# Performance work log

Measured on AMD Instinct MI355X. Metric: run time of the kernel, lower is better.

Reference implementation:

```python
import jax, jax.numpy as jnp
from jax import lax
import numpy as np

L = 4
KH, KW = 3, 3


def setup_inputs() -> dict:
    key = jax.random.key(0)
    k1, k2, k3, k4 = jax.random.split(key, 4)
    B, H, W, C = 32, 512, 512, 3
    inputs = jax.random.normal(k1, (B, H, W, C), dtype=jnp.float32)
    # posterior_loc ~ 'random_normal' initializer (stddev 0.05 in keras)
    posterior_loc = 0.05 * jax.random.normal(k2, (KH, KW, C, 1), dtype=jnp.float32)
    # posterior_scale initialized to constant -5.0 (small perturbation for non-degeneracy)
    posterior_scale = jnp.full((KH, KW, C, 1), -5.0, dtype=jnp.float32) + 0.1 * jax.random.normal(k3, (KH, KW, C, 1), dtype=jnp.float32)
    # reparameterization noise, one independent sample per pyramid level
    eps = jax.random.normal(k4, (L, KH, KW, C, 1), dtype=jnp.float32)
    return {"inputs": inputs, "posterior_loc": posterior_loc, "posterior_scale": posterior_scale, "eps": eps}


def _center_mask(dtype):
    # zero at the kernel center, one elsewhere (scatter of sampled values into non-center taps)
    m = np.ones((KH, KW, 1, 1), dtype=np.float32)
    m[KH // 2, KW // 2, 0, 0] = 0.0
    return jnp.asarray(m, dtype=dtype)


def _depthwise(x, kernel_hwc1):
    # x: [B,h,w,C], kernel_hwc1: [KH,KW,C,1] (TF depthwise layout) -> HWIO [KH,KW,1,C]
    C = x.shape[-1]
    k = jnp.transpose(kernel_hwc1, (0, 1, 3, 2))
    return lax.conv_general_dilated(
        x, k, window_strides=(1, 1), padding="SAME",
        dimension_numbers=("NHWC", "HWIO", "NHWC"), feature_group_count=C)


def reference(inputs, posterior_loc, posterior_scale, eps):
    B, H, W, C = inputs.shape
    sigma = jax.nn.softplus(posterior_scale)  # posterior stddev
    mask = _center_mask(inputs.dtype)
    total_error = jnp.zeros((B, H, W), dtype=inputs.dtype)
    for l in range(1, L + 1):
        factor = 2 ** (l - 1)
        th, tw = H // factor, W // factor
        ds = jax.image.resize(inputs, (B, th, tw, C), method="bilinear", antialias=True)
        # sampled Bayesian kernel: center tap zeroed, then normalized per channel
        v = posterior_loc + sigma * eps[l - 1]
        kern = v * mask
        kern = kern / (jnp.sum(kern, axis=(0, 1), keepdims=True) + 1e-7)
        r_hat = _depthwise(ds, kern)
        err = ds - r_hat
        up = jax.image.resize(err, (B, H, W, C), method="bilinear", antialias=False)
        total_error = total_error + jnp.sum(up, axis=-1)
    recon = jnp.mean(jnp.sum(jnp.square(total_error), axis=(1, 2)))
    # KL(N(mu, sigma) || N(0,1)), summed; added once per conv call -> L times
    kl = jnp.sum(-jnp.log(sigma) + 0.5 * (jnp.square(sigma) + jnp.square(posterior_loc)) - 0.5)
    return recon + L * kl
```

## Files before the change

kernel.cpp:

```cpp
#include <hip/hip_runtime.h>
#include <hip/hip_fp16.h>
#include <math.h>

#define BB 32
#define HH 512
#define WW 512
#define CC 3
#define LL 4

static __device__ __forceinline__ float softplusf_(float x) {
    if (x > 20.f) return x;
    return log1pf(expf(x));
}
static __device__ __forceinline__ int iclamp_(int v, int lo, int hi) {
    return v < lo ? lo : (v > hi ? hi : v);
}

__global__ void prep_kernel(const float* __restrict__ loc, const float* __restrict__ scale,
                            const float* __restrict__ eps, float* __restrict__ knorm,
                            double* __restrict__ kl_out) {
    int tid = threadIdx.x;
    float klv = 0.f;
    if (tid < 27) {
        float s = softplusf_(scale[tid]);
        float m = loc[tid];
        klv = -logf(s) + 0.5f * (s * s + m * m) - 0.5f;
    }
    #pragma unroll
    for (int off = 32; off; off >>= 1) klv += __shfl_down(klv, off);
    if (tid == 0) *kl_out = (double)klv;
    if (tid < 12) {
        int l = tid / 3;
        int c = tid - l * 3;
        float v[9];
        float sum = 0.f;
        #pragma unroll
        for (int t = 0; t < 9; ++t) {
            int idx = t * 3 + c;
            float s = softplusf_(scale[idx]);
            float val = loc[idx] + s * eps[l * 27 + idx];
            if (t == 4) val = 0.f;
            v[t] = val;
            sum += val;
        }
        float denom = sum + 1e-7f;
        #pragma unroll
        for (int t = 0; t < 9; ++t)
            knorm[l * 27 + t * 3 + c] = v[t] / denom;
    }
}

#define SJ(j) ((j) + ((j) >> 5))
#define PSTRIDE 532
#define RESC 1.1428571428571428f

__global__ void hpass_kernel(const float* __restrict__ x, __half* __restrict__ xh2,
                             __half* __restrict__ xh4, __half* __restrict__ xh8) {
    __shared__ __align__(16) float planes[4 * 3 * PSTRIDE];
    const int tid = threadIdx.x;
    const int lane = tid & 63;
    const int wv = tid >> 6;
    const int bh = blockIdx.x * 4 + wv;
    float* pl = planes + wv * (3 * PSTRIDE);

    const float4* src = (const float4*)(x + bh * (WW * CC));
    #pragma unroll
    for (int s = 0; s < 6; ++s) {
        int i = lane + (s << 6);
        float4 v = src[i];
        int g = i << 2;
        int j = g / 3;
        int c = g - j * 3;
        float e[4] = {v.x, v.y, v.z, v.w};
        #pragma unroll
        for (int u = 0; u < 4; ++u) {
            pl[c * PSTRIDE + SJ(j)] = e[u];
            ++c;
            if (c == 3) { c = 0; ++j; }
        }
    }
    asm volatile("s_waitcnt lgkmcnt(0)" ::: "memory");

    if (xh2) {
        const float W2k[4] = {0.125f, 0.375f, 0.375f, 0.125f};
        __half* o2 = xh2 + bh * 768;
        #pragma unroll
        for (int s = 0; s < 4; ++s) {
            int ow = lane + (s << 6);
            int j0 = 2 * ow - 1;
            bool edge = (j0 < 0) | (j0 + 3 > 511);
            float sc = edge ? RESC : 1.f;
            float wk[4]; int jj[4];
            #pragma unroll
            for (int k = 0; k < 4; ++k) {
                int j = j0 + k;
                wk[k] = (((unsigned)j < 512u) ? W2k[k] : 0.f) * sc;
                jj[k] = SJ(iclamp_(j, 0, 511));
            }
            #pragma unroll
            for (int c = 0; c < 3; ++c) {
                const float* p = pl + c * PSTRIDE;
                float a = 0.f;
                #pragma unroll
                for (int k = 0; k < 4; ++k) a += wk[k] * p[jj[k]];
                o2[ow * 3 + c] = __float2half_rn(a);
            }
        }
    }
    if (xh4) {
        const float W4k[8] = {0.03125f, 0.09375f, 0.15625f, 0.21875f,
                              0.21875f, 0.15625f, 0.09375f, 0.03125f};
        __half* o4 = xh4 + bh * 384;
        #pragma unroll
        for (int s = 0; s < 2; ++s) {
            int ow = lane + (s << 6);
            int j0 = 4 * ow - 2;
            bool edge = (j0 < 0) | (j0 + 7 > 511);
            float sc = edge ? RESC : 1.f;
            float wk[8]; int jj[8];
            #pragma unroll
            for (int k = 0; k < 8; ++k) {
                int j = j0 + k;
                wk[k] = (((unsigned)j < 512u) ? W4k[k] : 0.f) * sc;
                jj[k] = SJ(iclamp_(j, 0, 511));
            }
            #pragma unroll
            for (int c = 0; c < 3; ++c) {
                const float* p = pl + c * PSTRIDE;
                float a = 0.f;
                #pragma unroll
                for (int k = 0; k < 8; ++k) a += wk[k] * p[jj[k]];
                o4[ow * 3 + c] = __float2half_rn(a);
            }
        }
    }
    if (xh8) {
        const float W8k[16] = {0.0078125f, 0.0234375f, 0.0390625f, 0.0546875f,
                               0.0703125f, 0.0859375f, 0.1015625f, 0.1171875f,
                               0.1171875f, 0.1015625f, 0.0859375f, 0.0703125f,
                               0.0546875f, 0.0390625f, 0.0234375f, 0.0078125f};
        __half* o8 = xh8 + bh * 192;
        int ow = lane;
        int j0 = 8 * ow - 4;
        bool edge = (j0 < 0) | (j0 + 15 > 511);
        float sc = edge ? RESC : 1.f;
        float wk[16]; int jj[16];
        #pragma unroll
        for (int k = 0; k < 16; ++k) {
            int j = j0 + k;
            wk[k] = (((unsigned)j < 512u) ? W8k[k] : 0.f) * sc;
            jj[k] = SJ(iclamp_(j, 0, 511));
        }
        #pragma unroll
        for (int c = 0; c < 3; ++c) {
            const float* p = pl + c * PSTRIDE;
            float a = 0.f;
            #pragma unroll
            for (int k = 0; k < 16; ++k) a += wk[k] * p[jj[k]];
            o8[ow * 3 + c] = __float2half_rn(a);
        }
    }
}

template <int F, int THB>
static __device__ __forceinline__ void level_body(const __half* __restrict__ xh,
                                                  const float* __restrict__ knorm_all, int lvl,
                                                  float* __restrict__ es, int bx, int by, int b,
                                                  char* smem_raw) {
    constexpr int TH = HH / F, TW = WW / F, TW3 = TW * 3, TAPS = 2 * F;
    constexpr int RS = (THB + 3) * F;
    constexpr int DR = THB + 2;
    __half* stg = (__half*)smem_raw;
    float* dst = (float*)(smem_raw + RS * 108 * 2);
    float* wvv = dst + DR * 108;
    float* kn = wvv + DR * TAPS;
    int owb = bx * 32, ohb = by * THB;
    int tid = threadIdx.x;
    if (tid < 27) kn[tid] = knorm_all[lvl * 27 + tid];
    if (tid >= 32 && tid < 32 + DR) {
        int r = tid - 32;
        int oh = ohb - 1 + r;
        if (oh < 0 || oh >= TH) {
            #pragma unroll
            for (int k = 0; k < TAPS; ++k) wvv[r * TAPS + k] = 0.f;
        } else {
            float sfh = (oh + 0.5f) * F - 0.5f;
            int j0 = oh * F - F / 2;
            float tmp[TAPS]; float s = 0.f;
            #pragma unroll
            for (int k = 0; k < TAPS; ++k) {
                int j = j0 + k;
                float w = (j >= 0 && j < HH) ? (1.f - fabsf(j - sfh) * (1.0f / F)) : 0.f;
                tmp[k] = w; s += w;
            }
            float inv = 1.f / s;
            #pragma unroll
            for (int k = 0; k < TAPS; ++k) wvv[r * TAPS + k] = tmp[k] * inv;
        }
    }
    int jmin = (ohb - 1) * F - F / 2;
    int cb = owb * 3 - 4;
    bool fast = (cb >= 0) && (cb + 108 <= TW3);
    const __half* xb = xh + b * (HH * TW3);
    for (int i = tid; i < RS * 27; i += 256) {
        int r = i / 27;
        int c4 = (i - r * 27) * 4;
        int jh = iclamp_(jmin + r, 0, HH - 1);
        const __half* rp = xb + jh * TW3;
        if (fast) {
            *(ushort4*)&stg[r * 108 + c4] = *(const ushort4*)(rp + cb + c4);
        } else {
            #pragma unroll
            for (int u = 0; u < 4; ++u) {
                int col = iclamp_(cb + c4 + u, 0, TW3 - 1);
                stg[r * 108 + c4 + u] = rp[col];
            }
        }
    }
    __syncthreads();
    for (int i = tid; i < DR * 27; i += 256) {
        int r = i / 27;
        int c4 = (i - r * 27) * 4;
        int gc = cb + c4;
        float v0 = 0, v1 = 0, v2 = 0, v3 = 0;
        if ((unsigned)gc < (unsigned)TW3) {
            const __half* sp = &stg[r * F * 108 + c4];
            const float* wr = &wvv[r * TAPS];
            #pragma unroll
            for (int k = 0; k < TAPS; ++k) {
                float wk = wr[k];
                const __half2* h2 = (const __half2*)(sp + k * 108);
                float2 f0 = __half22float2(h2[0]);
                float2 f1 = __half22float2(h2[1]);
                v0 += wk * f0.x; v1 += wk * f0.y;
                v2 += wk * f1.x; v3 += wk * f1.y;
            }
        }
        float4 q; q.x = v0; q.y = v1; q.z = v2; q.w = v3;
        *(float4*)&dst[r * 108 + c4] = q;
    }
    __syncthreads();
    for (int i = tid; i < THB * 32; i += 256) {
        int wl = i & 31, hl = i >> 5;
        int base = hl * 108 + wl * 3 + 1;
        float e = 0.f;
        #pragma unroll
        for (int c = 0; c < 3; ++c) {
            float conv = 0.f;
            #pragma unroll
            for (int dh = 0; dh < 3; ++dh)
                #pragma unroll
                for (int dw = 0; dw < 3; ++dw)
                    conv += kn[(dh * 3 + dw) * 3 + c] * dst[base + dh * 108 + dw * 3 + c];
            e += dst[base + 108 + 3 + c] - conv;
        }
        es[b * (TH * TW) + (ohb + hl) * TW + owb + wl] = e;
    }
}

__global__ void levels_kernel(const __half* __restrict__ xh2, const __half* __restrict__ xh4,
                              const __half* __restrict__ xh8, const float* __restrict__ knorm,
                              float* __restrict__ es2, float* __restrict__ es3,
                              float* __restrict__ es4, int block_base) {
    __shared__ __align__(16) char smem[16896];
    int vb = blockIdx.x + block_base;
    if (vb < 4096) {
        level_body<2, 16>(xh2, knorm, 1, es2, vb & 7, (vb >> 3) & 15, vb >> 7, smem);
    } else if (vb < 6144) {
        int l = vb - 4096;
        level_body<4, 8>(xh4, knorm, 2, es3, l & 3, (l >> 2) & 15, l >> 6, smem);
    } else {
        int l = vb - 6144;
        level_body<8, 4>(xh8, knorm, 3, es4, l & 1, (l >> 1) & 15, l >> 5, smem);
    }
}

#define FPS 35
#define FPC (34 * FPS)
__global__ void __launch_bounds__(256, 8)
fused_kernel(const float* __restrict__ x, const float* __restrict__ knorm,
             const float* __restrict__ es2, const float* __restrict__ es3,
             const float* __restrict__ es4, double* __restrict__ partials) {
    __shared__ __align__(16) float planes[3 * FPC];
    __shared__ float e2t[18 * 19];
    __shared__ float e3t[10 * 11];
    __shared__ float e4t[6 * 7];
    __shared__ float kn[27];
    __shared__ float smf[4];
    int b = blockIdx.z;
    int hb = blockIdx.y * 32, wb = blockIdx.x * 32;
    int tid = threadIdx.x;
    if (tid < 27) kn[tid] = knorm[tid];
    const float* xb = x + b * (HH * WW * CC);
    int cb = wb * 3 - 4;
    bool fastc = (cb >= 0) && (cb + 108 <= WW * CC);
    for (int i = tid; i < 918; i += 256) {
        int r = i / 27;
        int f0 = (i - r * 27) * 4;
        int gh = hb - 1 + r;
        bool ghv = (unsigned)gh < (unsigned)HH;
        float vv[4] = {0.f, 0.f, 0.f, 0.f};
        if (ghv) {
            const float* rp = xb + gh * (WW * CC);
            if (fastc) {
                float4 v = *(const float4*)(rp + cb + f0);
                vv[0] = v.x; vv[1] = v.y; vv[2] = v.z; vv[3] = v.w;
            } else {
                int g0 = cb + f0;
                #pragma unroll
                for (int u = 0; u < 4; ++u)
                    vv[u] = ((unsigned)(g0 + u) < (unsigned)(WW * CC)) ? rp[g0 + u] : 0.f;
            }
        }
        #pragma unroll
        for (int u = 0; u < 4; ++u) {
            int f = f0 + u;
            if (f >= 1 && f <= 102) {
                int lc = (f - 1) / 3;
                int ch = (f - 1) - lc * 3;
                planes[ch * FPC + r * FPS + lc] = vv[u];
            }
        }
    }
    {
        const float* e2b = es2 + b * (256 * 256);
        int h0 = hb / 2 - 1, w0 = wb / 2 - 1;
        for (int i = tid; i < 18 * 32; i += 256) {
            int r = i >> 5, c = i & 31;
            if (c < 18) {
                int gh = iclamp_(h0 + r, 0, 255);
                int gw = iclamp_(w0 + c, 0, 255);
                e2t[r * 19 + c] = e2b[gh * 256 + gw];
            }
        }
        const float* e3b = es3 + b * (128 * 128);
        int h03 = hb / 4 - 1, w03 = wb / 4 - 1;
        if (tid < 160) {
            int r = tid >> 4, c = tid & 15;
            if (c < 10) {
                int gh = iclamp_(h03 + r, 0, 127);
                int gw = iclamp_(w03 + c, 0, 127);
                e3t[r * 11 + c] = e3b[gh * 128 + gw];
            }
        }
        const float* e4b = es4 + b * (64 * 64);
        int h04 = hb / 8 - 1, w04 = wb / 8 - 1;
        if (tid < 48) {
            int r = tid >> 3, c = tid & 7;
            if (c < 6) {
                int gh = iclamp_(h04 + r, 0, 63);
                int gw = iclamp_(w04 + c, 0, 63);
                e4t[r * 7 + c] = e4b[gh * 64 + gw];
            }
        }
    }
    __syncthreads();

    int q = tid >> 3;
    int a = tid & 7;
    float cv0 = 0, cv1 = 0, cv2 = 0, cv3 = 0;
    float ce0 = 0, ce1 = 0, ce2 = 0, ce3 = 0;
    #pragma unroll
    for (int c = 0; c < 3; ++c) {
        const float* P = planes + c * FPC;
        #pragma unroll
        for (int dh = 0; dh < 3; ++dh) {
            const float* r0 = P + (q + dh) * FPS + 4 * a;
            float w0 = r0[0], w1 = r0[1], w2 = r0[2], w3 = r0[3], w4 = r0[4], w5 = r0[5];
            float ka = kn[dh * 9 + c], kb = kn[dh * 9 + 3 + c], kc = kn[dh * 9 + 6 + c];
            cv0 += ka * w0 + kb * w1 + kc * w2;
            cv1 += ka * w1 + kb * w2 + kc * w3;
            cv2 += ka * w2 + kb * w3 + kc * w4;
            cv3 += ka * w3 + kb * w4 + kc * w5;
            if (dh == 1) { ce0 += w1; ce1 += w2; ce2 += w3; ce3 += w4; }
        }
    }
    float e[4] = {ce0 - cv0, ce1 - cv1, ce2 - cv2, ce3 - cv3};

    int n2 = q & 1;   float fh2 = n2 ? 0.25f : 0.75f;               int rh2 = (q >> 1) + n2;
    int n4 = q & 3;   float fh4 = ((n4 + 2) & 3) * 0.25f + 0.125f;  int rh4 = (q >> 2) + (n4 < 2 ? 0 : 1);
    int n8 = q & 7;   float fh8 = ((n8 + 4) & 7) * 0.125f + 0.0625f; int rh8 = (q >> 3) + (n8 < 4 ? 0 : 1);
    {
        const float* r0 = &e2t[rh2 * 19 + 2 * a];
        const float* r1 = r0 + 19;
        float t0 = r0[0], t1 = r0[1], t2 = r0[2], t3 = r0[3];
        float b0 = r1[0], b1 = r1[1], b2 = r1[2], b3 = r1[3];
        float top, bot;
        top = t0 + 0.75f * (t1 - t0); bot = b0 + 0.75f * (b1 - b0); e[0] += top + fh2 * (bot - top);
        top = t1 + 0.25f * (t2 - t1); bot = b1 + 0.25f * (b2 - b1); e[1] += top + fh2 * (bot - top);
        top = t1 + 0.75f * (t2 - t1); bot = b1 + 0.75f * (b2 - b1); e[2] += top + fh2 * (bot - top);
        top = t2 + 0.25f * (t3 - t2); bot = b2 + 0.25f * (b3 - b2); e[3] += top + fh2 * (bot - top);
    }
    {
        const float* r0 = &e3t[rh4 * 11 + a];
        const float* r1 = r0 + 11;
        float t0 = r0[0], t1 = r0[1], t2 = r0[2];
        float b0 = r1[0], b1 = r1[1], b2 = r1[2];
        float top, bot;
        top = t0 + 0.625f * (t1 - t0); bot = b0 + 0.625f * (b1 - b0); e[0] += top + fh4 * (bot - top);
        top = t0 + 0.875f * (t1 - t0); bot = b0 + 0.875f * (b1 - b0); e[1] += top + fh4 * (bot - top);
        top = t1 + 0.125f * (t2 - t1); bot = b1 + 0.125f * (b2 - b1); e[2] += top + fh4 * (bot - top);
        top = t1 + 0.375f * (t2 - t1); bot = b1 + 0.375f * (b2 - b1); e[3] += top + fh4 * (bot - top);
    }
    {
        int rw8 = (a >> 1) + (a & 1);
        const float* r0 = &e4t[rh8 * 7 + rw8];
        const float* r1 = r0 + 7;
        float t0 = r0[0], t1 = r0[1];
        float b0 = r1[0], b1 = r1[1];
        float fwb = (a & 1) ? 0.0625f : 0.5625f;
        #pragma unroll
        for (int p = 0; p < 4; ++p) {
            float fw = fwb + 0.125f * p;
            float top = t0 + fw * (t1 - t0);
            float bot = b0 + fw * (b1 - b0);
            e[p] += top + fh8 * (bot - top);
        }
    }
    float acc = e[0] * e[0] + e[1] * e[1] + e[2] * e[2] + e[3] * e[3];
    #pragma unroll
    for (int off = 32; off; off >>= 1) acc += __shfl_down(acc, off);
    if ((tid & 63) == 0) smf[tid >> 6] = acc;
    __syncthreads();
    if (tid == 0) {
        double s = (double)smf[0] + (double)smf[1] + (double)smf[2] + (double)smf[3];
        partials[(b * 16 + blockIdx.y) * 16 + blockIdx.x] = s;
    }
}

__global__ void final_kernel(const double* __restrict__ partials, int n,
                             const double* __restrict__ kl, float* __restrict__ out) {
    __shared__ double sm[1024];
    double acc = 0.0;
    for (int i = threadIdx.x; i < n; i += 1024) acc += partials[i];
    sm[threadIdx.x] = acc;
    __syncthreads();
    for (int s = 512; s > 0; s >>= 1) {
        if (threadIdx.x < (unsigned)s) sm[threadIdx.x] += sm[threadIdx.x + s];
        __syncthreads();
    }
    if (threadIdx.x == 0) out[0] = (float)(sm[0] / (double)BB + (double)LL * kl[0]);
}

extern "C" void kernel_launch(void* const* d_in, const int* in_sizes, int n_in,
                              void* d_out, int out_size, void* d_ws, size_t ws_size,
                              hipStream_t stream) {
    const float* x = (const float*)d_in[0];
    const float* loc = (const float*)d_in[1];
    const float* scale = (const float*)d_in[2];
    const float* eps = (const float*)d_in[3];
    float* out = (float*)d_out;

    char* ws = (char*)d_ws;
    float* knorm = (float*)(ws + 0);
    double* kl = (double*)(ws + 512);
    double* partials = (double*)(ws + 1024);
    float* es4 = (float*)(ws + 131072);
    float* es3 = (float*)(ws + 655360);
    float* es2 = (float*)(ws + 2752512);
    (void)in_sizes; (void)n_in; (void)out_size;

    prep_kernel<<<1, 64, 0, stream>>>(loc, scale, eps, knorm, kl);

    const size_t SINGLE_NEED = 55181312ull;
    if (ws_size >= SINGLE_NEED) {
        __half* xh2 = (__half*)(ws + 11141120);
        __half* xh4 = (__half*)(ws + 36306944);
        __half* xh8 = (__half*)(ws + 48889856);
        hpass_kernel<<<BB * HH / 4, 256, 0, stream>>>(x, xh2, xh4, xh8);
        levels_kernel<<<7168, 256, 0, stream>>>(xh2, xh4, xh8, knorm, es2, es3, es4, 0);
    } else {
        __half* xh4 = (__half*)(ws + 11141120);
        __half* xh8 = (__half*)(ws + 23724032);
        __half* xh2 = (__half*)(ws + 11141120);
        hpass_kernel<<<BB * HH / 4, 256, 0, stream>>>(x, nullptr, xh4, xh8);
        levels_kernel<<<3072, 256, 0, stream>>>(nullptr, xh4, xh8, knorm, es2, es3, es4, 4096);
        hpass_kernel<<<BB * HH / 4, 256, 0, stream>>>(x, xh2, nullptr, nullptr);
        levels_kernel<<<4096, 256, 0, stream>>>(xh2, nullptr, nullptr, knorm, es2, es3, es4, 0);
    }

    fused_kernel<<<dim3(16, 16, BB), 256, 0, stream>>>(x, knorm, es2, es3, es4, partials);
    final_kernel<<<1, 1024, 0, stream>>>(partials, 8192, kl, out);
}
```

Measured before the change: 109.6 us.

## Load full-res conv window directly from global; widen level staging loads to 16B

The fused kernel no longer stages the full-resolution input tile into shared-memory channel planes. Each thread now reads its 3x3 neighborhood rows straight from global memory with float4 loads and computes the depthwise conv in registers. This removes a large shared-memory allocation and a transposing scatter, which should raise occupancy, at the cost of redundant global and L2 reads across neighboring rows. The levels kernel staging also moves from 8-byte to 16-byte loads, with the row pitch padded to 112 halves and realigned offsets.

```diff
diff --git a/kernel.cpp b/kernel.cpp
--- a/kernel.cpp
+++ b/kernel.cpp
@@ -171,7 +171,7 @@
     constexpr int RS = (THB + 3) * F;
     constexpr int DR = THB + 2;
     __half* stg = (__half*)smem_raw;
-    float* dst = (float*)(smem_raw + RS * 108 * 2);
+    float* dst = (float*)(smem_raw + RS * 112 * 2);
     float* wvv = dst + DR * 108;
     float* kn = wvv + DR * TAPS;
     int owb = bx * 32, ohb = by * THB;
@@ -200,20 +200,21 @@
     }
     int jmin = (ohb - 1) * F - F / 2;
     int cb = owb * 3 - 4;
-    bool fast = (cb >= 0) && (cb + 108 <= TW3);
+    int cb2 = cb - 4;
+    bool fast = (cb2 >= 0) && (cb2 + 112 <= TW3);
     const __half* xb = xh + b * (HH * TW3);
-    for (int i = tid; i < RS * 27; i += 256) {
-        int r = i / 27;
-        int c4 = (i - r * 27) * 4;
+    for (int i = tid; i < RS * 14; i += 256) {
+        int r = i / 14;
+        int c8 = (i - r * 14) * 8;
         int jh = iclamp_(jmin + r, 0, HH - 1);
         const __half* rp = xb + jh * TW3;
         if (fast) {
-            *(ushort4*)&stg[r * 108 + c4] = *(const ushort4*)(rp + cb + c4);
+            *(uint4*)&stg[r * 112 + c8] = *(const uint4*)(rp + cb2 + c8);
         } else {
             #pragma unroll
-            for (int u = 0; u < 4; ++u) {
-                int col = iclamp_(cb + c4 + u, 0, TW3 - 1);
-                stg[r * 108 + c4 + u] = rp[col];
+            for (int u = 0; u < 8; ++u) {
+                int col = iclamp_(cb2 + c8 + u, 0, TW3 - 1);
+                stg[r * 112 + c8 + u] = rp[col];
             }
         }
     }
@@ -224,12 +225,12 @@
         int gc = cb + c4;
         float v0 = 0, v1 = 0, v2 = 0, v3 = 0;
         if ((unsigned)gc < (unsigned)TW3) {
-            const __half* sp = &stg[r * F * 108 + c4];
+            const __half* sp = &stg[r * F * 112 + c4 + 4];
             const float* wr = &wvv[r * TAPS];
             #pragma unroll
             for (int k = 0; k < TAPS; ++k) {
                 float wk = wr[k];
-                const __half2* h2 = (const __half2*)(sp + k * 108);
+                const __half2* h2 = (const __half2*)(sp + k * 112);
                 float2 f0 = __half22float2(h2[0]);
                 float2 f1 = __half22float2(h2[1]);
                 v0 += wk * f0.x; v1 += wk * f0.y;
@@ -275,13 +276,9 @@
     }
 }
 
-#define FPS 35
-#define FPC (34 * FPS)
-__global__ void __launch_bounds__(256, 8)
-fused_kernel(const float* __restrict__ x, const float* __restrict__ knorm,
-             const float* __restrict__ es2, const float* __restrict__ es3,
-             const float* __restrict__ es4, double* __restrict__ partials) {
-    __shared__ __align__(16) float planes[3 * FPC];
+__global__ void fused_kernel(const float* __restrict__ x, const float* __restrict__ knorm,
+                             const float* __restrict__ es2, const float* __restrict__ es3,
+                             const float* __restrict__ es4, double* __restrict__ partials) {
     __shared__ float e2t[18 * 19];
     __shared__ float e3t[10 * 11];
     __shared__ float e4t[6 * 7];
@@ -291,37 +288,6 @@
     int hb = blockIdx.y * 32, wb = blockIdx.x * 32;
     int tid = threadIdx.x;
     if (tid < 27) kn[tid] = knorm[tid];
-    const float* xb = x + b * (HH * WW * CC);
-    int cb = wb * 3 - 4;
-    bool fastc = (cb >= 0) && (cb + 108 <= WW * CC);
-    for (int i = tid; i < 918; i += 256) {
-        int r = i / 27;
-        int f0 = (i - r * 27) * 4;
-        int gh = hb - 1 + r;
-        bool ghv = (unsigned)gh < (unsigned)HH;
-        float vv[4] = {0.f, 0.f, 0.f, 0.f};
-        if (ghv) {
-            const float* rp = xb + gh * (WW * CC);
-            if (fastc) {
-                float4 v = *(const float4*)(rp + cb + f0);
-                vv[0] = v.x; vv[1] = v.y; vv[2] = v.z; vv[3] = v.w;
-            } else {
-                int g0 = cb + f0;
-                #pragma unroll
-                for (int u = 0; u < 4; ++u)
-                    vv[u] = ((unsigned)(g0 + u) < (unsigned)(WW * CC)) ? rp[g0 + u] : 0.f;
-            }
-        }
-        #pragma unroll
-        for (int u = 0; u < 4; ++u) {
-            int f = f0 + u;
-            if (f >= 1 && f <= 102) {
-                int lc = (f - 1) / 3;
-                int ch = (f - 1) - lc * 3;
-                planes[ch * FPC + r * FPS + lc] = vv[u];
-            }
-        }
-    }
     {
         const float* e2b = es2 + b * (256 * 256);
         int h0 = hb / 2 - 1, w0 = wb / 2 - 1;
@@ -358,21 +324,49 @@
 
     int q = tid >> 3;
     int a = tid & 7;
+    const float* xb = x + b * (HH * WW * CC);
+    bool le = (wb + 4 * a == 0);
+    bool re = (wb + 4 * a + 4 == WW);
+    int cwb = wb * 3 + 12 * a - 4;
+
     float cv0 = 0, cv1 = 0, cv2 = 0, cv3 = 0;
     float ce0 = 0, ce1 = 0, ce2 = 0, ce3 = 0;
     #pragma unroll
-    for (int c = 0; c < 3; ++c) {
-        const float* P = planes + c * FPC;
-        #pragma unroll
-        for (int dh = 0; dh < 3; ++dh) {
-            const float* r0 = P + (q + dh) * FPS + 4 * a;
-            float w0 = r0[0], w1 = r0[1], w2 = r0[2], w3 = r0[3], w4 = r0[4], w5 = r0[5];
-            float ka = kn[dh * 9 + c], kb = kn[dh * 9 + 3 + c], kc = kn[dh * 9 + 6 + c];
-            cv0 += ka * w0 + kb * w1 + kc * w2;
-            cv1 += ka * w1 + kb * w2 + kc * w3;
-            cv2 += ka * w2 + kb * w3 + kc * w4;
-            cv3 += ka * w3 + kb * w4 + kc * w5;
-            if (dh == 1) { ce0 += w1; ce1 += w2; ce2 += w3; ce3 += w4; }
+    for (int dh = 0; dh < 3; ++dh) {
+        int gh = hb + q - 1 + dh;
+        if ((unsigned)gh < (unsigned)HH) {
+            const float* rp = xb + gh * (WW * CC) + cwb;
+            float W[20];
+            if (!le) {
+                float4 t = *(const float4*)(rp);
+                W[0] = t.x; W[1] = t.y; W[2] = t.z; W[3] = t.w;
+            } else { W[0] = W[1] = W[2] = W[3] = 0.f; }
+            #pragma unroll
+            for (int j = 1; j < 4; ++j) {
+                float4 t = *(const float4*)(rp + 4 * j);
+                W[4 * j + 0] = t.x; W[4 * j + 1] = t.y; W[4 * j + 2] = t.z; W[4 * j + 3] = t.w;
+            }
+            if (!re) {
+                float4 t = *(const float4*)(rp + 16);
+                W[16] = t.x; W[17] = t.y; W[18] = t.z; W[19] = t.w;
+            } else { W[16] = W[17] = W[18] = W[19] = 0.f; }
+            #pragma unroll
+            for (int dw = 0; dw < 3; ++dw) {
+                #pragma unroll
+                for (int c = 0; c < 3; ++c) {
+                    float k = kn[(dh * 3 + dw) * 3 + c];
+                    cv0 += k * W[3 * 0 + 3 * dw + c + 1];
+                    cv1 += k * W[3 * 1 + 3 * dw + c + 1];
+                    cv2 += k * W[3 * 2 + 3 * dw + c + 1];
+                    cv3 += k * W[3 * 3 + 3 * dw + c + 1];
+                }
+            }
+            if (dh == 1) {
+                ce0 += W[4] + W[5] + W[6];
+                ce1 += W[7] + W[8] + W[9];
+                ce2 += W[10] + W[11] + W[12];
+                ce3 += W[13] + W[14] + W[15];
+            }
         }
     }
     float e[4] = {ce0 - cv0, ce1 - cv1, ce2 - cv2, ce3 - cv3};
```

Result: slower. 116.8 us (+6.6%).
